# Kernel optimization log

Hardware: AMD Instinct MI355X
Metric: run time of the kernel (lower is better)

The kernel has to match this reference:

```python
import jax, jax.numpy as jnp
import numpy as np

DIM = 128
H = 8
HD = DIM // H
NL = 6
DFF = 2048
EPS = 1e-5
S2S_STEPS = 6


def _ln(x, g, b):
    m = jnp.mean(x, -1, keepdims=True)
    v = jnp.mean(jnp.square(x - m), -1, keepdims=True)
    return (x - m) / jnp.sqrt(v + EPS) * g + b


def _lstm_step(x, h, c, wih, whh, bih, bhh):
    # torch LSTM gate order: i, f, g, o
    gates = x @ wih.T + bih + h @ whh.T + bhh
    i, f, g, o = jnp.split(gates, 4, axis=-1)
    c = jax.nn.sigmoid(f) * c + jax.nn.sigmoid(i) * jnp.tanh(g)
    h = jax.nn.sigmoid(o) * jnp.tanh(c)
    return h, c


def setup_inputs() -> dict:
    key = jax.random.key(0)
    ks = iter(jax.random.split(key, 16))
    n = lambda shape: jax.random.normal(next(ks), shape, jnp.float32) * 0.02
    inp = {
        "data": jax.random.normal(next(ks), (64, 256, 3), jnp.float32),
        "lin0_w": n((DIM, 3)), "lin0_b": jnp.zeros((DIM,), jnp.float32),
        "attn_in_w": n((NL, 3 * DIM, DIM)), "attn_in_b": jnp.zeros((NL, 3 * DIM), jnp.float32),
        "attn_out_w": n((NL, DIM, DIM)), "attn_out_b": jnp.zeros((NL, DIM), jnp.float32),
        "ln1_g": jnp.ones((NL, DIM), jnp.float32), "ln1_b": jnp.zeros((NL, DIM), jnp.float32),
        "ff_w1": n((NL, DFF, DIM)), "ff_b1": jnp.zeros((NL, DFF), jnp.float32),
        "ff_w2": n((NL, DIM, DFF)), "ff_b2": jnp.zeros((NL, DIM), jnp.float32),
        "ln2_g": jnp.ones((NL, DIM), jnp.float32), "ln2_b": jnp.zeros((NL, DIM), jnp.float32),
        "s2s_wih": n((4 * DIM, 2 * DIM)), "s2s_whh": n((4 * DIM, DIM)),
        "s2s_bih": jnp.zeros((4 * DIM,), jnp.float32), "s2s_bhh": jnp.zeros((4 * DIM,), jnp.float32),
        "mem_wih": n((4 * DIM, 2 * DIM)), "mem_whh": n((4 * DIM, DIM)),
        "mem_bih": jnp.zeros((4 * DIM,), jnp.float32), "mem_bhh": jnp.zeros((4 * DIM,), jnp.float32),
        "lin1_w": n((DIM, DIM)), "lin1_b": jnp.zeros((DIM,), jnp.float32),
        "lin3_w": n((1, DIM)), "lin3_b": jnp.zeros((1,), jnp.float32),
    }
    return inp


def reference(data, lin0_w, lin0_b, attn_in_w, attn_in_b, attn_out_w, attn_out_b,
              ln1_g, ln1_b, ff_w1, ff_b1, ff_w2, ff_b2, ln2_g, ln2_b,
              s2s_wih, s2s_whh, s2s_bih, s2s_bhh,
              mem_wih, mem_whh, mem_bih, mem_bhh,
              lin1_w, lin1_b, lin3_w, lin3_b):
    x = jax.nn.relu(data @ lin0_w.T + lin0_b)  # [S=64, B=256, D]
    S, B, _ = x.shape
    # torch TransformerEncoder with batch_first=False: attention over axis 0,
    # axis 1 is the transformer batch. Post-norm layers (norm_first=False), relu FFN.
    for l in range(NL):
        qkv = x @ attn_in_w[l].T + attn_in_b[l]
        q, k, v = jnp.split(qkv, 3, axis=-1)
        q = q.reshape(S, B, H, HD)
        k = k.reshape(S, B, H, HD)
        v = v.reshape(S, B, H, HD)
        scores = jnp.einsum('sbhd,tbhd->bhst', q, k) / np.float32(np.sqrt(HD))
        attn = jax.nn.softmax(scores, axis=-1)
        ao = jnp.einsum('bhst,tbhd->sbhd', attn, v).reshape(S, B, DIM)
        x = _ln(x + ao @ attn_out_w[l].T + attn_out_b[l], ln1_g[l], ln1_b[l])
        ff = jax.nn.relu(x @ ff_w1[l].T + ff_b1[l]) @ ff_w2[l].T + ff_b2[l]
        x = _ln(x + ff, ln2_g[l], ln2_b[l])
    # Set2Set pooling: bidxs assign segment = axis-0 index for each block of
    # num_atoms consecutive rows of flatten(out,0,1), i.e. pool over axis 1.
    q_star = jnp.zeros((S, 2 * DIM), x.dtype)
    h = jnp.zeros((S, DIM), x.dtype)
    c = jnp.zeros((S, DIM), x.dtype)
    for _ in range(S2S_STEPS):
        h, c = _lstm_step(q_star, h, c, s2s_wih, s2s_whh, s2s_bih, s2s_bhh)
        e = jnp.einsum('bnd,bd->bn', x, h)          # [S, num_atoms]
        a = jax.nn.softmax(e, axis=-1)              # segment softmax (uniform segs)
        r = jnp.einsum('bn,bnd->bd', a, x)          # segment weighted sum
        q_star = jnp.concatenate([h, r], axis=-1)   # [S, 2D]
    # memory LSTM: seq_len 1, zero initial state (states=None branch)
    hx = jnp.zeros((S, DIM), x.dtype)
    cx = jnp.zeros((S, DIM), x.dtype)
    hx, cx = _lstm_step(q_star, hx, cx, mem_wih, mem_whh, mem_bih, mem_bhh)
    o = jax.nn.relu(hx @ lin1_w.T + lin1_b)
    v_out = (o @ lin3_w.T + lin3_b)[None]  # [1, S, 1]
    return v_out, hx[None], cx[None]
```

## Files before the change

kernel.cpp:

```cpp
#include <hip/hip_runtime.h>
#include <math.h>


typedef _Float16 __attribute__((ext_vector_type(8))) f16x8;
typedef __attribute__((ext_vector_type(4))) float f32x4;
typedef _Float16 __attribute__((ext_vector_type(2))) h16x2;

__device__ __forceinline__ unsigned short f2h(float f) {
  union { _Float16 h; unsigned short s; } x; x.h = (_Float16)f; return x.s;
}
__device__ __forceinline__ float h2f(unsigned short u) {
  union { unsigned short s; _Float16 h; } x; x.s = u; return (float)x.h;
}
__device__ __forceinline__ unsigned packh(float a, float b) {
  return (unsigned)f2h(a) | ((unsigned)f2h(b) << 16);
}
__device__ __forceinline__ float hlo(unsigned u) {
  union { unsigned short s; _Float16 h; } x; x.s = (unsigned short)(u & 0xffff);
  return (float)x.h;
}
__device__ __forceinline__ float hhi(unsigned u) {
  union { unsigned short s; _Float16 h; } x; x.s = (unsigned short)(u >> 16);
  return (float)x.h;
}
__device__ __forceinline__ float fdot2u(unsigned a, unsigned b, float c) {
#if __has_builtin(__builtin_amdgcn_fdot2)
  union U { unsigned u; h16x2 h; };
  U x, y; x.u = a; y.u = b;
  return __builtin_amdgcn_fdot2(x.h, y.h, c, false);
#else
  return c + hlo(a) * hlo(b) + hhi(a) * hhi(b);
#endif
}
__device__ __forceinline__ float sigf(float x) { return 1.f / (1.f + expf(-x)); }

__device__ __forceinline__ void gl2lds16(const void* g, void* l) {
  __builtin_amdgcn_global_load_lds(
      (const __attribute__((address_space(1))) unsigned int*)g,
      (__attribute__((address_space(3))) unsigned int*)l, 16, 0, 0);
}

__global__ __launch_bounds__(256) void convw_kernel(
    const float* __restrict__ aiw, const float* __restrict__ aow,
    const float* __restrict__ w1, const float* __restrict__ w2,
    const float* __restrict__ wih, const float* __restrict__ whh,
    const float* __restrict__ mwih,
    unsigned short* __restrict__ o0, unsigned short* __restrict__ o1,
    unsigned short* __restrict__ o2, unsigned short* __restrict__ o3,
    unsigned short* __restrict__ o4, unsigned short* __restrict__ o5,
    unsigned short* __restrict__ o6) {
  int i = blockIdx.x * 256 + threadIdx.x;
  if (i < 294912) {
    int l = i / 49152, o = i % 49152;
    int j = o & 7, fr = (o >> 3) & 15, fq = (o >> 7) & 3, ks = (o >> 9) & 3,
        rb = o >> 11;
    o0[i] = f2h(aiw[l * 49152 + (rb * 16 + fr) * 128 + ks * 32 + fq * 8 + j]);
  } else if (i < 393216) {
    int ii = i - 294912;
    int l = ii / 16384, o = ii % 16384;
    int j = o & 7, fr = (o >> 3) & 15, fq = (o >> 7) & 3, ks = (o >> 9) & 3,
        rb = o >> 11;
    o1[ii] = f2h(aow[l * 16384 + (rb * 16 + fr) * 128 + ks * 32 + fq * 8 + j]);
  } else if (i < 1966080) {
    int ii = i - 393216;
    int l = ii >> 18, o = ii & 262143;
    int j = o & 7, fr = (o >> 3) & 15, fq = (o >> 7) & 3, ks = (o >> 9) & 3,
        rb = o >> 11;
    o2[ii] = f2h(w1[l * 262144 + (rb * 16 + fr) * 128 + ks * 32 + fq * 8 + j]);
  } else if (i < 3538944) {
    int ii = i - 1966080;
    int l = ii >> 18, o = ii & 262143;
    int j = o & 7, fr = (o >> 3) & 15, fq = (o >> 7) & 3, ks = (o >> 9) & 63,
        rb = o >> 15;
    o3[ii] = f2h(w2[l * 262144 + (rb * 16 + fr) * 2048 + ks * 32 + fq * 8 + j]);
  } else if (i < 3670016) {
    int j = i - 3538944; o4[j] = f2h(wih[j]);
  } else if (i < 3735552) {
    int j = i - 3670016; o5[j] = f2h(whh[j]);
  } else {
    int j = i - 3735552; o6[j] = f2h(mwih[j]);
  }
}

__global__ __launch_bounds__(256) void lin0_kernel(
    const float* __restrict__ data, const float* __restrict__ w,
    const float* __restrict__ b, float* __restrict__ x,
    unsigned short* __restrict__ xb) {
  int i = blockIdx.x * 256 + threadIdx.x;
  int n = i >> 7, d = i & 127;
  float v = b[d] + data[n * 3 + 0] * w[d * 3 + 0]
                 + data[n * 3 + 1] * w[d * 3 + 1]
                 + data[n * 3 + 2] * w[d * 3 + 2];
  v = fmaxf(v, 0.0f);
  x[i] = v;
  xb[i] = f2h(v);
}

__global__ __launch_bounds__(512) void qkv_kernel(
    const unsigned short* __restrict__ xbg,
    const unsigned short* __restrict__ wqkv, const float* __restrict__ bqkv,
    unsigned short* __restrict__ qkvg) {
  __shared__ __align__(16) unsigned short Xs[8192];
  __shared__ __align__(16) unsigned short img[24576];

  int tid = threadIdx.x, w = tid >> 6, lane = tid & 63;
  int b = blockIdx.x;
  int r4 = lane >> 4, cs = lane & 15;
  int fr = lane & 15, fq = lane >> 4;

#pragma unroll
  for (int i = 0; i < 2; i++) {
    int issue = w * 2 + i;
    int row = issue * 4 + r4;
    int g = cs ^ (row & 7);
    gl2lds16(xbg + (size_t)(row * 256 + b) * 128 + g * 8,
             (char*)Xs + issue * 1024);
  }
  __syncthreads();

  f32x4 acc[4][3];
#pragma unroll
  for (int i = 0; i < 4; i++)
#pragma unroll
    for (int j = 0; j < 3; j++) acc[i][j] = (f32x4){0.f, 0.f, 0.f, 0.f};
#pragma unroll
  for (int ks = 0; ks < 4; ks++) {
    f16x8 bf[3];
#pragma unroll
    for (int ni = 0; ni < 3; ni++)
      bf[ni] = *(const f16x8*)(wqkv + (size_t)(w * 3 + ni) * 2048 + ks * 512 +
                               fq * 128 + fr * 8);
    f16x8 af[4];
#pragma unroll
    for (int mi = 0; mi < 4; mi++) {
      int row = mi * 16 + fr;
      int kq = (ks * 4 + fq) ^ (row & 7);
      af[mi] = *(const f16x8*)(Xs + row * 128 + kq * 8);
    }
#pragma unroll
    for (int mi = 0; mi < 4; mi++)
#pragma unroll
      for (int ni = 0; ni < 3; ni++)
        acc[mi][ni] = __builtin_amdgcn_mfma_f32_16x16x32_f16(
            af[mi], bf[ni], acc[mi][ni], 0, 0, 0);
  }
#pragma unroll
  for (int ni = 0; ni < 3; ni++) {
    int c = (w * 3 + ni) * 16 + fr;
    float bv = bqkv[c];
    if (c < 128) {
#pragma unroll
      for (int mi = 0; mi < 4; mi++)
#pragma unroll
        for (int r = 0; r < 4; r++) {
          int row = mi * 16 + fq * 4 + r;
          int prow = row & 31;
          img[(row >> 5) * 4096 + prow * 128 +
              (((c >> 3) ^ (prow & 7)) << 3) + (c & 7)] =
              f2h(acc[mi][ni][r] + bv);
        }
    } else if (c < 256) {
      int cc = c - 128;
#pragma unroll
      for (int mi = 0; mi < 4; mi++)
#pragma unroll
        for (int r = 0; r < 4; r++) {
          int row = mi * 16 + fq * 4 + r;
          img[8192 + row * 128 + (((cc >> 3) ^ (row & 7)) << 3) + (cc & 7)] =
              f2h(acc[mi][ni][r] + bv);
        }
    } else {
      int f = c - 256;
#pragma unroll
      for (int mi = 0; mi < 4; mi++)
#pragma unroll
        for (int r = 0; r < 4; r++) {
          int srow = mi * 16 + fq * 4 + r;
          img[16384 + f * 64 + (((srow >> 3) ^ (f & 7)) << 3) + (srow & 7)] =
              f2h(acc[mi][ni][r] + bv);
        }
    }
  }
  __syncthreads();

  const uint4* s4 = (const uint4*)img;
  uint4* d4 = (uint4*)(qkvg + (size_t)b * 24576);
#pragma unroll
  for (int i = 0; i < 6; i++) d4[i * 512 + tid] = s4[i * 512 + tid];
}

__global__ __launch_bounds__(256, 3) void layer_kernel(
    const unsigned short* __restrict__ qkvg,
    const unsigned short* __restrict__ wout, const float* __restrict__ bout,
    const float* __restrict__ ln1g, const float* __restrict__ ln1b,
    const unsigned short* __restrict__ w1, const float* __restrict__ b1,
    const unsigned short* __restrict__ w2, const float* __restrict__ b2,
    const float* __restrict__ ln2g, const float* __restrict__ ln2b,
    float* __restrict__ xio, unsigned short* __restrict__ xbo) {
  __shared__ __align__(16) unsigned short SM[20480];
  __shared__ float psum[4][32], psq[4][32];
  __shared__ float2 stats[32];
  __shared__ __align__(16) uint4 zchunk;

  unsigned short* Qs = SM;
  unsigned short* Ks = SM + 4096;
  unsigned short* VT = SM + 12288;
  unsigned short* AOs = SM + 12288;
  unsigned short* Xn = SM;

  int tid = threadIdx.x, w = tid >> 6, lane = tid & 63;
  int b = blockIdx.x >> 1, half = blockIdx.x & 1;
  int fr = lane & 15, fq = lane >> 4;

  if (tid == 0) zchunk = make_uint4(0u, 0u, 0u, 0u);

  const unsigned short* src = qkvg + (size_t)b * 24576;
#pragma unroll
  for (int i = 0; i < 10; i++) {
    int l = w * 10 + i;
    int soff = (l < 8 ? half * 4096 : 4096) + l * 512;
    gl2lds16(src + soff + lane * 8, (char*)SM + l * 1024);
  }
  __syncthreads();

  f32x4 po[2][2];
#pragma unroll
  for (int i = 0; i < 2; i++)
#pragma unroll
    for (int j = 0; j < 2; j++) po[i][j] = (f32x4){0.f, 0.f, 0.f, 0.f};
  {
    f16x8 afH[2][2], bfH[2][4];
#pragma unroll
    for (int hi = 0; hi < 2; hi++) {
      int h = w * 2 + hi;
#pragma unroll
      for (int mi2 = 0; mi2 < 2; mi2++) {
        int qrow = mi2 * 16 + fr;
        const unsigned short* pa =
            (fq < 2) ? (Qs + qrow * 128 + (((h * 2 + fq) ^ (qrow & 7)) << 3))
                     : (const unsigned short*)&zchunk;
        afH[hi][mi2] = *(const f16x8*)pa;
      }
#pragma unroll
      for (int ti = 0; ti < 4; ti++) {
        int trow = ti * 16 + fr;
        const unsigned short* pb =
            (fq < 2) ? (Ks + trow * 128 + (((h * 2 + fq) ^ (trow & 7)) << 3))
                     : (const unsigned short*)&zchunk;
        bfH[hi][ti] = *(const f16x8*)pb;
      }
    }
    __syncthreads();

    unsigned short* Pb = Ks + w * 2048;
#pragma unroll
    for (int hi = 0; hi < 2; hi++) {
      int h = w * 2 + hi;
      f32x4 sc[2][4];
#pragma unroll
      for (int i = 0; i < 2; i++)
#pragma unroll
        for (int j = 0; j < 4; j++) sc[i][j] = (f32x4){0.f, 0.f, 0.f, 0.f};
#pragma unroll
      for (int mi2 = 0; mi2 < 2; mi2++)
#pragma unroll
        for (int ti = 0; ti < 4; ti++)
          sc[mi2][ti] = __builtin_amdgcn_mfma_f32_16x16x32_f16(
              afH[hi][mi2], bfH[hi][ti], sc[mi2][ti], 0, 0, 0);
#pragma unroll
      for (int mi2 = 0; mi2 < 2; mi2++) {
#pragma unroll
        for (int r = 0; r < 4; r++) {
          float m = -1e30f;
#pragma unroll
          for (int ti = 0; ti < 4; ti++) m = fmaxf(m, sc[mi2][ti][r]);
          m = fmaxf(m, __shfl_xor(m, 1, 64));
          m = fmaxf(m, __shfl_xor(m, 2, 64));
          m = fmaxf(m, __shfl_xor(m, 4, 64));
          m = fmaxf(m, __shfl_xor(m, 8, 64));
          m *= 0.25f;
          float ss = 0.f;
#pragma unroll
          for (int ti = 0; ti < 4; ti++) {
            float p = expf(sc[mi2][ti][r] * 0.25f - m);
            sc[mi2][ti][r] = p;
            ss += p;
          }
          ss += __shfl_xor(ss, 1, 64);
          ss += __shfl_xor(ss, 2, 64);
          ss += __shfl_xor(ss, 4, 64);
          ss += __shfl_xor(ss, 8, 64);
          float inv = 1.f / ss;
          int prow = mi2 * 16 + fq * 4 + r;
#pragma unroll
          for (int ti = 0; ti < 4; ti++) {
            int t = ti * 16 + fr;
            Pb[prow * 64 + (((t >> 3) ^ (prow & 7)) << 3) + (t & 7)] =
                f2h(sc[mi2][ti][r] * inv);
          }
        }
      }
#pragma unroll
      for (int ks2 = 0; ks2 < 2; ks2++) {
        f16x8 af[2], bf;
#pragma unroll
        for (int si2 = 0; si2 < 2; si2++) {
          int prow = si2 * 16 + fr;
          int kq = (ks2 * 4 + fq) ^ (prow & 7);
          af[si2] = *(const f16x8*)(Pb + prow * 64 + kq * 8);
        }
        {
          int vrow = h * 16 + fr;
          int kq = (ks2 * 4 + fq) ^ (vrow & 7);
          bf = *(const f16x8*)(VT + vrow * 64 + kq * 8);
        }
#pragma unroll
        for (int si2 = 0; si2 < 2; si2++)
          po[hi][si2] = __builtin_amdgcn_mfma_f32_16x16x32_f16(
              af[si2], bf, po[hi][si2], 0, 0, 0);
      }
    }
  }
  __syncthreads();
#pragma unroll
  for (int hi = 0; hi < 2; hi++) {
    int c = (w * 2 + hi) * 16 + fr;
#pragma unroll
    for (int si2 = 0; si2 < 2; si2++)
#pragma unroll
      for (int r = 0; r < 4; r++) {
        int arow = si2 * 16 + fq * 4 + r;
        AOs[arow * 128 + (((c >> 3) ^ (arow & 7)) << 3) + (c & 7)] =
            f2h(po[hi][si2][r]);
      }
  }
  __syncthreads();

  {
    f32x4 acc[2][2];
#pragma unroll
    for (int i = 0; i < 2; i++)
#pragma unroll
      for (int j = 0; j < 2; j++) acc[i][j] = (f32x4){0.f, 0.f, 0.f, 0.f};
#pragma unroll
    for (int ks = 0; ks < 4; ks++) {
      f16x8 af[2], bwo[2];
#pragma unroll
      for (int si2 = 0; si2 < 2; si2++) {
        int rowl = si2 * 16 + fr;
        int kq = (ks * 4 + fq) ^ (rowl & 7);
        af[si2] = *(const f16x8*)(AOs + rowl * 128 + kq * 8);
      }
#pragma unroll
      for (int ni = 0; ni < 2; ni++)
        bwo[ni] = *(const f16x8*)(wout + (size_t)(w * 2 + ni) * 2048 +
                                  ks * 512 + fq * 128 + fr * 8);
#pragma unroll
      for (int si2 = 0; si2 < 2; si2++)
#pragma unroll
        for (int ni = 0; ni < 2; ni++)
          acc[si2][ni] = __builtin_amdgcn_mfma_f32_16x16x32_f16(
              af[si2], bwo[ni], acc[si2][ni], 0, 0, 0);
    }
    float vv4[2][2][4];
    float sums[2][4], sqs[2][4];
#pragma unroll
    for (int si2 = 0; si2 < 2; si2++)
#pragma unroll
      for (int r = 0; r < 4; r++) { sums[si2][r] = 0.f; sqs[si2][r] = 0.f; }
#pragma unroll
    for (int ni = 0; ni < 2; ni++) {
      int c = (w * 2 + ni) * 16 + fr;
      float bv = bout[c];
#pragma unroll
      for (int si2 = 0; si2 < 2; si2++)
#pragma unroll
        for (int r = 0; r < 4; r++) {
          int rowl = si2 * 16 + fq * 4 + r;
          int rowg = half * 32 + rowl;
          float v = acc[si2][ni][r] + bv +
                    xio[(size_t)(rowg * 256 + b) * 128 + c];
          vv4[ni][si2][r] = v;
          sums[si2][r] += v;
          sqs[si2][r] += v * v;
        }
    }
#pragma unroll
    for (int d = 1; d < 16; d <<= 1) {
#pragma unroll
      for (int si2 = 0; si2 < 2; si2++)
#pragma unroll
        for (int r = 0; r < 4; r++) {
          sums[si2][r] += __shfl_xor(sums[si2][r], d, 64);
          sqs[si2][r] += __shfl_xor(sqs[si2][r], d, 64);
        }
    }
    if (fr == 0) {
#pragma unroll
      for (int si2 = 0; si2 < 2; si2++)
#pragma unroll
        for (int r = 0; r < 4; r++) {
          int rowl = si2 * 16 + fq * 4 + r;
          psum[w][rowl] = sums[si2][r];
          psq[w][rowl] = sqs[si2][r];
        }
    }
    __syncthreads();
    if (tid < 32) {
      float S = 0.f, Q = 0.f;
#pragma unroll
      for (int ww = 0; ww < 4; ww++) { S += psum[ww][tid]; Q += psq[ww][tid]; }
      float m = S * (1.f / 128.f);
      float var = Q * (1.f / 128.f) - m * m;
      stats[tid] = make_float2(m, rsqrtf(var + 1e-5f));
    }
    __syncthreads();
#pragma unroll
    for (int ni = 0; ni < 2; ni++) {
      int c = (w * 2 + ni) * 16 + fr;
      float gl = ln1g[c], bl = ln1b[c];
#pragma unroll
      for (int si2 = 0; si2 < 2; si2++)
#pragma unroll
        for (int r = 0; r < 4; r++) {
          int rowl = si2 * 16 + fq * 4 + r;
          float2 st2 = stats[rowl];
          float y = (vv4[ni][si2][r] - st2.x) * st2.y * gl + bl;
          Xn[rowl * 128 + (((c >> 3) ^ (rowl & 7)) << 3) + (c & 7)] = f2h(y);
        }
    }
  }
  __syncthreads();

  f16x8 xfragF[4][2];
#pragma unroll
  for (int ks = 0; ks < 4; ks++)
#pragma unroll
    for (int mi2 = 0; mi2 < 2; mi2++) {
      int rowl = mi2 * 16 + fr;
      int kq = (ks * 4 + fq) ^ (rowl & 7);
      xfragF[ks][mi2] = *(const f16x8*)(Xn + rowl * 128 + kq * 8);
    }

  unsigned short* HsB = Ks;
  f32x4 acc2[2][2];
#pragma unroll
  for (int i = 0; i < 2; i++)
#pragma unroll
    for (int j = 0; j < 2; j++) acc2[i][j] = (f32x4){0.f, 0.f, 0.f, 0.f};

  for (int c = 0; c < 16; c++) {
    unsigned short* Hcur = HsB + (c & 1) * 4096;
    f32x4 acc1[2][2];
#pragma unroll
    for (int i = 0; i < 2; i++)
#pragma unroll
      for (int j = 0; j < 2; j++) acc1[i][j] = (f32x4){0.f, 0.f, 0.f, 0.f};
#pragma unroll
    for (int ks = 0; ks < 4; ks++) {
      f16x8 b1f[2];
#pragma unroll
      for (int ni = 0; ni < 2; ni++)
        b1f[ni] = *(const f16x8*)(w1 + (size_t)(c * 8 + w * 2 + ni) * 2048 +
                                  ks * 512 + fq * 128 + fr * 8);
#pragma unroll
      for (int mi2 = 0; mi2 < 2; mi2++)
#pragma unroll
        for (int ni = 0; ni < 2; ni++)
          acc1[mi2][ni] = __builtin_amdgcn_mfma_f32_16x16x32_f16(
              xfragF[ks][mi2], b1f[ni], acc1[mi2][ni], 0, 0, 0);
    }
#pragma unroll
    for (int ni = 0; ni < 2; ni++) {
      int col = (w * 2 + ni) * 16 + fr;
      float bv = b1[c * 128 + col];
#pragma unroll
      for (int mi2 = 0; mi2 < 2; mi2++)
#pragma unroll
        for (int r = 0; r < 4; r++) {
          int rowl = mi2 * 16 + fq * 4 + r;
          Hcur[rowl * 128 + (((col >> 3) ^ (rowl & 7)) << 3) + (col & 7)] =
              f2h(fmaxf(acc1[mi2][ni][r] + bv, 0.f));
        }
    }
    __syncthreads();
#pragma unroll
    for (int ks = 0; ks < 4; ks++) {
      f16x8 af[2], b2f[2];
#pragma unroll
      for (int si2 = 0; si2 < 2; si2++) {
        int rowl = si2 * 16 + fr;
        int kq = (ks * 4 + fq) ^ (rowl & 7);
        af[si2] = *(const f16x8*)(Hcur + rowl * 128 + kq * 8);
      }
#pragma unroll
      for (int ni = 0; ni < 2; ni++)
        b2f[ni] = *(const f16x8*)(w2 + (size_t)(w * 2 + ni) * 32768 +
                                  (c * 4 + ks) * 512 + fq * 128 + fr * 8);
#pragma unroll
      for (int si2 = 0; si2 < 2; si2++)
#pragma unroll
        for (int ni = 0; ni < 2; ni++)
          acc2[si2][ni] = __builtin_amdgcn_mfma_f32_16x16x32_f16(
              af[si2], b2f[ni], acc2[si2][ni], 0, 0, 0);
    }
  }

  {
    float vvo[2][2][4];
    float sums[2][4], sqs[2][4];
#pragma unroll
    for (int si2 = 0; si2 < 2; si2++)
#pragma unroll
      for (int r = 0; r < 4; r++) { sums[si2][r] = 0.f; sqs[si2][r] = 0.f; }
#pragma unroll
    for (int ni = 0; ni < 2; ni++) {
      int c = (w * 2 + ni) * 16 + fr;
      float bv = b2[c];
#pragma unroll
      for (int si2 = 0; si2 < 2; si2++)
#pragma unroll
        for (int r = 0; r < 4; r++) {
          int rowl = si2 * 16 + fq * 4 + r;
          float resid =
              h2f(Xn[rowl * 128 + (((c >> 3) ^ (rowl & 7)) << 3) + (c & 7)]);
          float v = acc2[si2][ni][r] + bv + resid;
          vvo[ni][si2][r] = v;
          sums[si2][r] += v;
          sqs[si2][r] += v * v;
        }
    }
#pragma unroll
    for (int d = 1; d < 16; d <<= 1) {
#pragma unroll
      for (int si2 = 0; si2 < 2; si2++)
#pragma unroll
        for (int r = 0; r < 4; r++) {
          sums[si2][r] += __shfl_xor(sums[si2][r], d, 64);
          sqs[si2][r] += __shfl_xor(sqs[si2][r], d, 64);
        }
    }
    if (fr == 0) {
#pragma unroll
      for (int si2 = 0; si2 < 2; si2++)
#pragma unroll
        for (int r = 0; r < 4; r++) {
          int rowl = si2 * 16 + fq * 4 + r;
          psum[w][rowl] = sums[si2][r];
          psq[w][rowl] = sqs[si2][r];
        }
    }
    __syncthreads();
    if (tid < 32) {
      float S = 0.f, Q = 0.f;
#pragma unroll
      for (int ww = 0; ww < 4; ww++) { S += psum[ww][tid]; Q += psq[ww][tid]; }
      float m = S * (1.f / 128.f);
      float var = Q * (1.f / 128.f) - m * m;
      stats[tid] = make_float2(m, rsqrtf(var + 1e-5f));
    }
    __syncthreads();
#pragma unroll
    for (int ni = 0; ni < 2; ni++) {
      int c = (w * 2 + ni) * 16 + fr;
      float gl = ln2g[c], bl = ln2b[c];
#pragma unroll
      for (int si2 = 0; si2 < 2; si2++)
#pragma unroll
        for (int r = 0; r < 4; r++) {
          int rowl = si2 * 16 + fq * 4 + r;
          float2 st = stats[rowl];
          float y = (vvo[ni][si2][r] - st.x) * st.y * gl + bl;
          size_t o = (size_t)((half * 32 + rowl) * 256 + b) * 128 + c;
          xio[o] = y;
          xbo[o] = f2h(y);
        }
    }
  }
}

__global__ __launch_bounds__(512, 1) void s2s_kernel(
    const unsigned short* __restrict__ xb,
    const unsigned short* __restrict__ wihh,
    const unsigned short* __restrict__ whhh,
    const float* __restrict__ bih, const float* __restrict__ bhh,
    const unsigned short* __restrict__ mwihh,
    const float* __restrict__ mbih, const float* __restrict__ mbhh,
    const float* __restrict__ l1w, const float* __restrict__ l1b,
    const float* __restrict__ l3w, const float* __restrict__ l3b,
    float* __restrict__ out) {
  __shared__ __align__(16) unsigned xl[256 * 65];
  __shared__ __align__(16) unsigned qu[128];
  __shared__ __align__(16) float cst[128];
  __shared__ __align__(16) float gates[512];
  __shared__ __align__(16) float red[256];
  __shared__ __align__(16) float aw[256];
  int s = blockIdx.x, t = threadIdx.x, lane = t & 63, w = t >> 6;

  uint4 wreg[32], ureg[16];
  {
    const uint4* wp = (const uint4*)(wihh + (size_t)t * 256);
#pragma unroll
    for (int i = 0; i < 32; i++) wreg[i] = wp[i];
    const uint4* up = (const uint4*)(whhh + (size_t)t * 128);
#pragma unroll
    for (int i = 0; i < 16; i++) ureg[i] = up[i];
  }

  const uint4* xs4 = (const uint4*)(xb + (size_t)s * 32768);
#pragma unroll
  for (int it = 0; it < 8; it++) {
    int f = it * 512 + t;
    uint4 v = xs4[f];
    int n = f >> 4, jc = (f & 15) * 4;
    unsigned* dst = xl + n * 65 + jc;
    dst[0] = v.x; dst[1] = v.y; dst[2] = v.z; dst[3] = v.w;
  }
  if (t < 128) cst[t] = 0.f;
  __syncthreads();

  const uint4* q4 = (const uint4*)qu;
  float bsum = bih[t] + bhh[t];

  for (int step = 0; step < 6; step++) {
    if (step > 0) {
      float a0 = 0.f, a1 = 0.f, a2 = 0.f, a3 = 0.f;
#pragma unroll
      for (int i = 0; i < 16; i++) {
        uint4 qv = q4[i];
        a0 = fdot2u(wreg[i].x, qv.x, a0);
        a1 = fdot2u(wreg[i].y, qv.y, a1);
        a2 = fdot2u(wreg[i].z, qv.z, a2);
        a3 = fdot2u(wreg[i].w, qv.w, a3);
        a0 = fdot2u(ureg[i].x, qv.x, a0);
        a1 = fdot2u(ureg[i].y, qv.y, a1);
        a2 = fdot2u(ureg[i].z, qv.z, a2);
        a3 = fdot2u(ureg[i].w, qv.w, a3);
      }
#pragma unroll
      for (int i = 16; i < 32; i++) {
        uint4 qv = q4[i];
        a0 = fdot2u(wreg[i].x, qv.x, a0);
        a1 = fdot2u(wreg[i].y, qv.y, a1);
        a2 = fdot2u(wreg[i].z, qv.z, a2);
        a3 = fdot2u(wreg[i].w, qv.w, a3);
      }
      gates[t] = bsum + ((a0 + a1) + (a2 + a3));
    } else {
      gates[t] = bsum;
    }
    __syncthreads();
    if (t < 128) {
      float ig = sigf(gates[t]), fg = sigf(gates[128 + t]);
      float gg = tanhf(gates[256 + t]), og = sigf(gates[384 + t]);
      float cn = fg * cst[t] + ig * gg;
      cst[t] = cn;
      float hn = og * tanhf(cn);
      float hp = __shfl_xor(hn, 1, 64);
      if ((t & 1) == 0) qu[t >> 1] = packh(hn, hp);
    }
    __syncthreads();
    if (step > 0) {
      int n = t >> 1, p = t & 1;
      const unsigned* xr = xl + n * 65 + p * 32;
      float e0 = 0.f, e1 = 0.f;
#pragma unroll 8
      for (int i = 0; i < 32; i += 2) {
        e0 = fdot2u(xr[i], qu[p * 32 + i], e0);
        e1 = fdot2u(xr[i + 1], qu[p * 32 + i + 1], e1);
      }
      float e = e0 + e1;
      e += __shfl_xor(e, 1, 64);
      if (p == 0) red[n] = e;
      __syncthreads();
      float v0 = red[lane], v1 = red[64 + lane];
      float v2 = red[128 + lane], v3 = red[192 + lane];
      float m = fmaxf(fmaxf(v0, v1), fmaxf(v2, v3));
#pragma unroll
      for (int d = 1; d < 64; d <<= 1) m = fmaxf(m, __shfl_xor(m, d, 64));
      float p0 = expf(v0 - m), p1 = expf(v1 - m);
      float p2 = expf(v2 - m), p3 = expf(v3 - m);
      float ss = p0 + p1 + p2 + p3;
#pragma unroll
      for (int d = 1; d < 64; d <<= 1) ss += __shfl_xor(ss, d, 64);
      float Sinv = 1.f / ss;
      if (w == 0) {
        aw[lane] = p0 * Sinv; aw[64 + lane] = p1 * Sinv;
        aw[128 + lane] = p2 * Sinv; aw[192 + lane] = p3 * Sinv;
      }
    } else {
      if (t < 256) aw[t] = 1.f / 256.f;
    }
    __syncthreads();
    {
      int d = t & 127, grp = t >> 7;
      const unsigned* xc = xl + grp * 64 * 65 + (d >> 1);
      int hi = d & 1;
      const float* ap = aw + grp * 64;
      float r = 0.f;
#pragma unroll 8
      for (int n2 = 0; n2 < 64; n2++) {
        unsigned u = xc[n2 * 65];
        r += ap[n2] * (hi ? hhi(u) : hlo(u));
      }
      gates[t] = r;
    }
    __syncthreads();
    if (t < 128) {
      float rd = gates[t] + gates[128 + t] + gates[256 + t] + gates[384 + t];
      float rp = __shfl_xor(rd, 1, 64);
      if ((t & 1) == 0) qu[64 + (t >> 1)] = packh(rd, rp);
    }
    __syncthreads();
  }
  {
    float a0 = 0.f, a1 = 0.f, a2 = 0.f, a3 = 0.f;
    const uint4* mp = (const uint4*)(mwihh + (size_t)t * 256);
#pragma unroll 8
    for (int i = 0; i < 32; i++) {
      uint4 wv = mp[i], qv = q4[i];
      a0 = fdot2u(wv.x, qv.x, a0);
      a1 = fdot2u(wv.y, qv.y, a1);
      a2 = fdot2u(wv.z, qv.z, a2);
      a3 = fdot2u(wv.w, qv.w, a3);
    }
    gates[t] = mbih[t] + mbhh[t] + ((a0 + a1) + (a2 + a3));
  }
  __syncthreads();
  if (t < 128) {
    float ig = sigf(gates[t]);
    float gg = tanhf(gates[256 + t]);
    float og = sigf(gates[384 + t]);
    float cx = ig * gg;
    float hx = og * tanhf(cx);
    cst[t] = hx;
    out[64 + s * 128 + t] = hx;
    out[64 + 8192 + s * 128 + t] = cx;
  }
  __syncthreads();
  if (t < 128) {
    float acc = l1b[t];
    const float4* w4 = (const float4*)(l1w + (size_t)t * 128);
    const float4* h4 = (const float4*)cst;
#pragma unroll 8
    for (int k = 0; k < 32; k++) {
      float4 a = w4[k], b = h4[k];
      acc += a.x * b.x + a.y * b.y + a.z * b.z + a.w * b.w;
    }
    red[t] = fmaxf(acc, 0.f) * l3w[t];
  } else if (t < 256) {
    red[t] = 0.f;
  }
  __syncthreads();
  for (int off = 128; off; off >>= 1) {
    if (t < off) red[t] += red[t + off];
    __syncthreads();
  }
  if (t == 0) out[s] = red[0] + l3b[0];
}

extern "C" void kernel_launch(void* const* d_in, const int* in_sizes, int n_in,
                              void* d_out, int out_size, void* d_ws,
                              size_t ws_size, hipStream_t stream) {
  const float* data       = (const float*)d_in[0];
  const float* lin0_w     = (const float*)d_in[1];
  const float* lin0_b     = (const float*)d_in[2];
  const float* attn_in_w  = (const float*)d_in[3];
  const float* attn_in_b  = (const float*)d_in[4];
  const float* attn_out_w = (const float*)d_in[5];
  const float* attn_out_b = (const float*)d_in[6];
  const float* ln1_g      = (const float*)d_in[7];
  const float* ln1_b      = (const float*)d_in[8];
  const float* ff_w1      = (const float*)d_in[9];
  const float* ff_b1      = (const float*)d_in[10];
  const float* ff_w2      = (const float*)d_in[11];
  const float* ff_b2      = (const float*)d_in[12];
  const float* ln2_g      = (const float*)d_in[13];
  const float* ln2_b      = (const float*)d_in[14];
  const float* s2s_wih    = (const float*)d_in[15];
  const float* s2s_whh    = (const float*)d_in[16];
  const float* s2s_bih    = (const float*)d_in[17];
  const float* s2s_bhh    = (const float*)d_in[18];
  const float* mem_wih    = (const float*)d_in[19];
  const float* mem_bih    = (const float*)d_in[21];
  const float* mem_bhh    = (const float*)d_in[22];
  const float* lin1_w     = (const float*)d_in[23];
  const float* lin1_b     = (const float*)d_in[24];
  const float* lin3_w     = (const float*)d_in[25];
  const float* lin3_b     = (const float*)d_in[26];
  float* out = (float*)d_out;

  char* p = (char*)d_ws;
  float* x = (float*)p;                      p += (size_t)16384 * 128 * 4;
  unsigned short* xb = (unsigned short*)p;   p += (size_t)16384 * 128 * 2;
  unsigned short* wqkv = (unsigned short*)p; p += (size_t)294912 * 2;
  unsigned short* wout = (unsigned short*)p; p += (size_t)98304 * 2;
  unsigned short* w1h = (unsigned short*)p;  p += (size_t)1572864 * 2;
  unsigned short* w2h = (unsigned short*)p;  p += (size_t)1572864 * 2;
  unsigned short* wihh = (unsigned short*)p; p += (size_t)131072 * 2;
  unsigned short* whhh = (unsigned short*)p; p += (size_t)65536 * 2;
  unsigned short* mwihh = (unsigned short*)p; p += (size_t)131072 * 2;
  unsigned short* qkvg = (unsigned short*)p; p += (size_t)256 * 24576 * 2;

  convw_kernel<<<15104, 256, 0, stream>>>(
      attn_in_w, attn_out_w, ff_w1, ff_w2, s2s_wih, s2s_whh, mem_wih,
      wqkv, wout, w1h, w2h, wihh, whhh, mwihh);
  lin0_kernel<<<8192, 256, 0, stream>>>(data, lin0_w, lin0_b, x, xb);

  for (int l = 0; l < 6; l++) {
    qkv_kernel<<<256, 512, 0, stream>>>(
        xb, wqkv + (size_t)l * 49152, attn_in_b + l * 384, qkvg);
    layer_kernel<<<512, 256, 0, stream>>>(
        qkvg,
        wout + (size_t)l * 16384, attn_out_b + l * 128,
        ln1_g + l * 128, ln1_b + l * 128,
        w1h + (size_t)l * 262144, ff_b1 + l * 2048,
        w2h + (size_t)l * 262144, ff_b2 + l * 128,
        ln2_g + l * 128, ln2_b + l * 128, x, xb);
  }

  s2s_kernel<<<64, 512, 0, stream>>>(
      xb, wihh, whhh, s2s_bih, s2s_bhh,
      mwihh, mem_bih, mem_bhh, lin1_w, lin1_b, lin3_w, lin3_b, out);
}
```

Baseline: 491.7 us.

## Fuse QKV projection into layer kernel and widen FFN hidden chunk

Removes the separate qkv_kernel and its global qkvg round-trip. Each layer block now loads its batch's 64 input rows and computes its own half of Q plus the full K and V in shared memory. Each block pair therefore recomputes K/V for the same batch, and LDS use grows, so occupancy drops from 3 to 2 blocks per SIMD bound. The FFN loop also processes 256-wide hidden chunks over 8 iterations instead of 128-wide over 16, halving barriers.

```diff
diff --git a/kernel.cpp b/kernel.cpp
--- a/kernel.cpp
+++ b/kernel.cpp
@@ -96,130 +96,166 @@
   xb[i] = f2h(v);
 }
 
-__global__ __launch_bounds__(512) void qkv_kernel(
+__global__ __launch_bounds__(256, 2) void layer_kernel(
     const unsigned short* __restrict__ xbg,
     const unsigned short* __restrict__ wqkv, const float* __restrict__ bqkv,
-    unsigned short* __restrict__ qkvg) {
-  __shared__ __align__(16) unsigned short Xs[8192];
-  __shared__ __align__(16) unsigned short img[24576];
-
-  int tid = threadIdx.x, w = tid >> 6, lane = tid & 63;
-  int b = blockIdx.x;
-  int r4 = lane >> 4, cs = lane & 15;
-  int fr = lane & 15, fq = lane >> 4;
-
-#pragma unroll
-  for (int i = 0; i < 2; i++) {
-    int issue = w * 2 + i;
-    int row = issue * 4 + r4;
-    int g = cs ^ (row & 7);
-    gl2lds16(xbg + (size_t)(row * 256 + b) * 128 + g * 8,
-             (char*)Xs + issue * 1024);
-  }
-  __syncthreads();
-
-  f32x4 acc[4][3];
-#pragma unroll
-  for (int i = 0; i < 4; i++)
-#pragma unroll
-    for (int j = 0; j < 3; j++) acc[i][j] = (f32x4){0.f, 0.f, 0.f, 0.f};
-#pragma unroll
-  for (int ks = 0; ks < 4; ks++) {
-    f16x8 bf[3];
-#pragma unroll
-    for (int ni = 0; ni < 3; ni++)
-      bf[ni] = *(const f16x8*)(wqkv + (size_t)(w * 3 + ni) * 2048 + ks * 512 +
-                               fq * 128 + fr * 8);
-    f16x8 af[4];
-#pragma unroll
-    for (int mi = 0; mi < 4; mi++) {
-      int row = mi * 16 + fr;
-      int kq = (ks * 4 + fq) ^ (row & 7);
-      af[mi] = *(const f16x8*)(Xs + row * 128 + kq * 8);
-    }
-#pragma unroll
-    for (int mi = 0; mi < 4; mi++)
-#pragma unroll
-      for (int ni = 0; ni < 3; ni++)
-        acc[mi][ni] = __builtin_amdgcn_mfma_f32_16x16x32_f16(
-            af[mi], bf[ni], acc[mi][ni], 0, 0, 0);
-  }
-#pragma unroll
-  for (int ni = 0; ni < 3; ni++) {
-    int c = (w * 3 + ni) * 16 + fr;
-    float bv = bqkv[c];
-    if (c < 128) {
-#pragma unroll
-      for (int mi = 0; mi < 4; mi++)
-#pragma unroll
-        for (int r = 0; r < 4; r++) {
-          int row = mi * 16 + fq * 4 + r;
-          int prow = row & 31;
-          img[(row >> 5) * 4096 + prow * 128 +
-              (((c >> 3) ^ (prow & 7)) << 3) + (c & 7)] =
-              f2h(acc[mi][ni][r] + bv);
-        }
-    } else if (c < 256) {
-      int cc = c - 128;
-#pragma unroll
-      for (int mi = 0; mi < 4; mi++)
-#pragma unroll
-        for (int r = 0; r < 4; r++) {
-          int row = mi * 16 + fq * 4 + r;
-          img[8192 + row * 128 + (((cc >> 3) ^ (row & 7)) << 3) + (cc & 7)] =
-              f2h(acc[mi][ni][r] + bv);
-        }
-    } else {
-      int f = c - 256;
-#pragma unroll
-      for (int mi = 0; mi < 4; mi++)
-#pragma unroll
-        for (int r = 0; r < 4; r++) {
-          int srow = mi * 16 + fq * 4 + r;
-          img[16384 + f * 64 + (((srow >> 3) ^ (f & 7)) << 3) + (srow & 7)] =
-              f2h(acc[mi][ni][r] + bv);
-        }
-    }
-  }
-  __syncthreads();
-
-  const uint4* s4 = (const uint4*)img;
-  uint4* d4 = (uint4*)(qkvg + (size_t)b * 24576);
-#pragma unroll
-  for (int i = 0; i < 6; i++) d4[i * 512 + tid] = s4[i * 512 + tid];
-}
-
-__global__ __launch_bounds__(256, 3) void layer_kernel(
-    const unsigned short* __restrict__ qkvg,
     const unsigned short* __restrict__ wout, const float* __restrict__ bout,
     const float* __restrict__ ln1g, const float* __restrict__ ln1b,
     const unsigned short* __restrict__ w1, const float* __restrict__ b1,
     const unsigned short* __restrict__ w2, const float* __restrict__ b2,
     const float* __restrict__ ln2g, const float* __restrict__ ln2b,
     float* __restrict__ xio, unsigned short* __restrict__ xbo) {
-  __shared__ __align__(16) unsigned short SM[20480];
+  __shared__ __align__(16) unsigned short SM[28672];
   __shared__ float psum[4][32], psq[4][32];
   __shared__ float2 stats[32];
   __shared__ __align__(16) uint4 zchunk;
 
-  unsigned short* Qs = SM;
-  unsigned short* Ks = SM + 4096;
-  unsigned short* VT = SM + 12288;
-  unsigned short* AOs = SM + 12288;
-  unsigned short* Xn = SM;
+  unsigned short* Xs = SM;
+  unsigned short* Ks = SM + 8192;
+  unsigned short* VT = SM + 16384;
+  unsigned short* AOs = SM + 16384;
+  unsigned short* Qs = SM + 24576;
+  unsigned short* Xn = SM + 24576;
 
   int tid = threadIdx.x, w = tid >> 6, lane = tid & 63;
   int b = blockIdx.x >> 1, half = blockIdx.x & 1;
+  int r4 = lane >> 4, cs = lane & 15;
   int fr = lane & 15, fq = lane >> 4;
 
   if (tid == 0) zchunk = make_uint4(0u, 0u, 0u, 0u);
 
-  const unsigned short* src = qkvg + (size_t)b * 24576;
-#pragma unroll
-  for (int i = 0; i < 10; i++) {
-    int l = w * 10 + i;
-    int soff = (l < 8 ? half * 4096 : 4096) + l * 512;
-    gl2lds16(src + soff + lane * 8, (char*)SM + l * 1024);
+#pragma unroll
+  for (int i = 0; i < 4; i++) {
+    int issue = w * 4 + i;
+    int row = issue * 4 + r4;
+    int g = cs ^ (row & 7);
+    gl2lds16(xbg + (size_t)(row * 256 + b) * 128 + g * 8,
+             (char*)Xs + issue * 1024);
+  }
+  __syncthreads();
+
+  {
+    f32x4 acc[2][2];
+#pragma unroll
+    for (int i = 0; i < 2; i++)
+#pragma unroll
+      for (int j = 0; j < 2; j++) acc[i][j] = (f32x4){0.f, 0.f, 0.f, 0.f};
+#pragma unroll
+    for (int ks = 0; ks < 4; ks++) {
+      f16x8 bf[2];
+#pragma unroll
+      for (int ni = 0; ni < 2; ni++)
+        bf[ni] = *(const f16x8*)(wqkv + (size_t)(w * 2 + ni) * 2048 +
+                                 ks * 512 + fq * 128 + fr * 8);
+      f16x8 af[2];
+#pragma unroll
+      for (int mi2 = 0; mi2 < 2; mi2++) {
+        int row = half * 32 + mi2 * 16 + fr;
+        int kq = (ks * 4 + fq) ^ (row & 7);
+        af[mi2] = *(const f16x8*)(Xs + row * 128 + kq * 8);
+      }
+#pragma unroll
+      for (int mi2 = 0; mi2 < 2; mi2++)
+#pragma unroll
+        for (int ni = 0; ni < 2; ni++)
+          acc[mi2][ni] = __builtin_amdgcn_mfma_f32_16x16x32_f16(
+              af[mi2], bf[ni], acc[mi2][ni], 0, 0, 0);
+    }
+#pragma unroll
+    for (int ni = 0; ni < 2; ni++) {
+      int c = (w * 2 + ni) * 16 + fr;
+      float bv = bqkv[c];
+#pragma unroll
+      for (int mi2 = 0; mi2 < 2; mi2++)
+#pragma unroll
+        for (int r = 0; r < 4; r++) {
+          int prow = mi2 * 16 + fq * 4 + r;
+          Qs[prow * 128 + (((c >> 3) ^ (prow & 7)) << 3) + (c & 7)] =
+              f2h(acc[mi2][ni][r] + bv);
+        }
+    }
+  }
+  {
+    f32x4 acc[4][2];
+#pragma unroll
+    for (int i = 0; i < 4; i++)
+#pragma unroll
+      for (int j = 0; j < 2; j++) acc[i][j] = (f32x4){0.f, 0.f, 0.f, 0.f};
+#pragma unroll
+    for (int ks = 0; ks < 4; ks++) {
+      f16x8 bf[2];
+#pragma unroll
+      for (int ni = 0; ni < 2; ni++)
+        bf[ni] = *(const f16x8*)(wqkv + (size_t)(8 + w * 2 + ni) * 2048 +
+                                 ks * 512 + fq * 128 + fr * 8);
+      f16x8 af[4];
+#pragma unroll
+      for (int mi = 0; mi < 4; mi++) {
+        int row = mi * 16 + fr;
+        int kq = (ks * 4 + fq) ^ (row & 7);
+        af[mi] = *(const f16x8*)(Xs + row * 128 + kq * 8);
+      }
+#pragma unroll
+      for (int mi = 0; mi < 4; mi++)
+#pragma unroll
+        for (int ni = 0; ni < 2; ni++)
+          acc[mi][ni] = __builtin_amdgcn_mfma_f32_16x16x32_f16(
+              af[mi], bf[ni], acc[mi][ni], 0, 0, 0);
+    }
+#pragma unroll
+    for (int ni = 0; ni < 2; ni++) {
+      int cc = (w * 2 + ni) * 16 + fr;
+      float bv = bqkv[128 + cc];
+#pragma unroll
+      for (int mi = 0; mi < 4; mi++)
+#pragma unroll
+        for (int r = 0; r < 4; r++) {
+          int row = mi * 16 + fq * 4 + r;
+          Ks[row * 128 + (((cc >> 3) ^ (row & 7)) << 3) + (cc & 7)] =
+              f2h(acc[mi][ni][r] + bv);
+        }
+    }
+  }
+  {
+    f32x4 acc[4][2];
+#pragma unroll
+    for (int i = 0; i < 4; i++)
+#pragma unroll
+      for (int j = 0; j < 2; j++) acc[i][j] = (f32x4){0.f, 0.f, 0.f, 0.f};
+#pragma unroll
+    for (int ks = 0; ks < 4; ks++) {
+      f16x8 bf[2];
+#pragma unroll
+      for (int ni = 0; ni < 2; ni++)
+        bf[ni] = *(const f16x8*)(wqkv + (size_t)(16 + w * 2 + ni) * 2048 +
+                                 ks * 512 + fq * 128 + fr * 8);
+      f16x8 af[4];
+#pragma unroll
+      for (int mi = 0; mi < 4; mi++) {
+        int row = mi * 16 + fr;
+        int kq = (ks * 4 + fq) ^ (row & 7);
+        af[mi] = *(const f16x8*)(Xs + row * 128 + kq * 8);
+      }
+#pragma unroll
+      for (int mi = 0; mi < 4; mi++)
+#pragma unroll
+        for (int ni = 0; ni < 2; ni++)
+          acc[mi][ni] = __builtin_amdgcn_mfma_f32_16x16x32_f16(
+              af[mi], bf[ni], acc[mi][ni], 0, 0, 0);
+    }
+#pragma unroll
+    for (int ni = 0; ni < 2; ni++) {
+      int f = (w * 2 + ni) * 16 + fr;
+      float bv = bqkv[256 + f];
+#pragma unroll
+      for (int mi = 0; mi < 4; mi++)
+#pragma unroll
+        for (int r = 0; r < 4; r++) {
+          int srow = mi * 16 + fq * 4 + r;
+          VT[f * 64 + (((srow >> 3) ^ (f & 7)) << 3) + (srow & 7)] =
+              f2h(acc[mi][ni][r] + bv);
+        }
+    }
   }
   __syncthreads();
 
@@ -229,17 +265,18 @@
 #pragma unroll
     for (int j = 0; j < 2; j++) po[i][j] = (f32x4){0.f, 0.f, 0.f, 0.f};
   {
-    f16x8 afH[2][2], bfH[2][4];
+    unsigned short* Pb = Xs + w * 2048;
 #pragma unroll
     for (int hi = 0; hi < 2; hi++) {
       int h = w * 2 + hi;
+      f16x8 afH[2], bfH[4];
 #pragma unroll
       for (int mi2 = 0; mi2 < 2; mi2++) {
         int qrow = mi2 * 16 + fr;
         const unsigned short* pa =
             (fq < 2) ? (Qs + qrow * 128 + (((h * 2 + fq) ^ (qrow & 7)) << 3))
                      : (const unsigned short*)&zchunk;
-        afH[hi][mi2] = *(const f16x8*)pa;
+        afH[mi2] = *(const f16x8*)pa;
       }
 #pragma unroll
       for (int ti = 0; ti < 4; ti++) {
@@ -247,15 +284,8 @@
         const unsigned short* pb =
             (fq < 2) ? (Ks + trow * 128 + (((h * 2 + fq) ^ (trow & 7)) << 3))
                      : (const unsigned short*)&zchunk;
-        bfH[hi][ti] = *(const f16x8*)pb;
-      }
-    }
-    __syncthreads();
-
-    unsigned short* Pb = Ks + w * 2048;
-#pragma unroll
-    for (int hi = 0; hi < 2; hi++) {
-      int h = w * 2 + hi;
+        bfH[ti] = *(const f16x8*)pb;
+      }
       f32x4 sc[2][4];
 #pragma unroll
       for (int i = 0; i < 2; i++)
@@ -266,7 +296,7 @@
 #pragma unroll
         for (int ti = 0; ti < 4; ti++)
           sc[mi2][ti] = __builtin_amdgcn_mfma_f32_16x16x32_f16(
-              afH[hi][mi2], bfH[hi][ti], sc[mi2][ti], 0, 0, 0);
+              afH[mi2], bfH[ti], sc[mi2][ti], 0, 0, 0);
 #pragma unroll
       for (int mi2 = 0; mi2 < 2; mi2++) {
 #pragma unroll
@@ -442,61 +472,60 @@
       xfragF[ks][mi2] = *(const f16x8*)(Xn + rowl * 128 + kq * 8);
     }
 
-  unsigned short* HsB = Ks;
   f32x4 acc2[2][2];
 #pragma unroll
   for (int i = 0; i < 2; i++)
 #pragma unroll
     for (int j = 0; j < 2; j++) acc2[i][j] = (f32x4){0.f, 0.f, 0.f, 0.f};
 
-  for (int c = 0; c < 16; c++) {
-    unsigned short* Hcur = HsB + (c & 1) * 4096;
-    f32x4 acc1[2][2];
+  for (int c = 0; c < 8; c++) {
+    unsigned short* Hcur = SM + (c & 1) * 8192;
+    f32x4 acc1[2][4];
 #pragma unroll
     for (int i = 0; i < 2; i++)
 #pragma unroll
-      for (int j = 0; j < 2; j++) acc1[i][j] = (f32x4){0.f, 0.f, 0.f, 0.f};
+      for (int j = 0; j < 4; j++) acc1[i][j] = (f32x4){0.f, 0.f, 0.f, 0.f};
 #pragma unroll
     for (int ks = 0; ks < 4; ks++) {
-      f16x8 b1f[2];
-#pragma unroll
-      for (int ni = 0; ni < 2; ni++)
-        b1f[ni] = *(const f16x8*)(w1 + (size_t)(c * 8 + w * 2 + ni) * 2048 +
+      f16x8 b1f[4];
+#pragma unroll
+      for (int ni = 0; ni < 4; ni++)
+        b1f[ni] = *(const f16x8*)(w1 + (size_t)(c * 16 + w * 4 + ni) * 2048 +
                                   ks * 512 + fq * 128 + fr * 8);
 #pragma unroll
       for (int mi2 = 0; mi2 < 2; mi2++)
 #pragma unroll
-        for (int ni = 0; ni < 2; ni++)
+        for (int ni = 0; ni < 4; ni++)
           acc1[mi2][ni] = __builtin_amdgcn_mfma_f32_16x16x32_f16(
               xfragF[ks][mi2], b1f[ni], acc1[mi2][ni], 0, 0, 0);
     }
 #pragma unroll
-    for (int ni = 0; ni < 2; ni++) {
-      int col = (w * 2 + ni) * 16 + fr;
-      float bv = b1[c * 128 + col];
+    for (int ni = 0; ni < 4; ni++) {
+      int col = (w * 4 + ni) * 16 + fr;
+      float bv = b1[c * 256 + col];
 #pragma unroll
       for (int mi2 = 0; mi2 < 2; mi2++)
 #pragma unroll
         for (int r = 0; r < 4; r++) {
           int rowl = mi2 * 16 + fq * 4 + r;
-          Hcur[rowl * 128 + (((col >> 3) ^ (rowl & 7)) << 3) + (col & 7)] =
+          Hcur[rowl * 256 + (((col >> 3) ^ (rowl & 7)) << 3) + (col & 7)] =
               f2h(fmaxf(acc1[mi2][ni][r] + bv, 0.f));
         }
     }
     __syncthreads();
 #pragma unroll
-    for (int ks = 0; ks < 4; ks++) {
+    for (int ks2 = 0; ks2 < 8; ks2++) {
       f16x8 af[2], b2f[2];
 #pragma unroll
       for (int si2 = 0; si2 < 2; si2++) {
         int rowl = si2 * 16 + fr;
-        int kq = (ks * 4 + fq) ^ (rowl & 7);
-        af[si2] = *(const f16x8*)(Hcur + rowl * 128 + kq * 8);
+        int kq = (ks2 * 4 + fq) ^ (rowl & 7);
+        af[si2] = *(const f16x8*)(Hcur + rowl * 256 + kq * 8);
       }
 #pragma unroll
       for (int ni = 0; ni < 2; ni++)
         b2f[ni] = *(const f16x8*)(w2 + (size_t)(w * 2 + ni) * 32768 +
-                                  (c * 4 + ks) * 512 + fq * 128 + fr * 8);
+                                  (c * 8 + ks2) * 512 + fq * 128 + fr * 8);
 #pragma unroll
       for (int si2 = 0; si2 < 2; si2++)
 #pragma unroll
@@ -800,7 +829,6 @@
   unsigned short* wihh = (unsigned short*)p; p += (size_t)131072 * 2;
   unsigned short* whhh = (unsigned short*)p; p += (size_t)65536 * 2;
   unsigned short* mwihh = (unsigned short*)p; p += (size_t)131072 * 2;
-  unsigned short* qkvg = (unsigned short*)p; p += (size_t)256 * 24576 * 2;
 
   convw_kernel<<<15104, 256, 0, stream>>>(
       attn_in_w, attn_out_w, ff_w1, ff_w2, s2s_wih, s2s_whh, mem_wih,
@@ -808,10 +836,8 @@
   lin0_kernel<<<8192, 256, 0, stream>>>(data, lin0_w, lin0_b, x, xb);
 
   for (int l = 0; l < 6; l++) {
-    qkv_kernel<<<256, 512, 0, stream>>>(
-        xb, wqkv + (size_t)l * 49152, attn_in_b + l * 384, qkvg);
     layer_kernel<<<512, 256, 0, stream>>>(
-        qkvg,
+        xb, wqkv + (size_t)l * 49152, attn_in_b + l * 384,
         wout + (size_t)l * 16384, attn_out_b + l * 128,
         ln1_g + l * 128, ln1_b + l * 128,
         w1h + (size_t)l * 262144, ff_b1 + l * 2048,
```

New measurement: 472.1 us. 4.0% less time.
